# Kernel optimization log

Measured on AMD Instinct MI355X. Metric: run time of the kernel, lower is better.

Reference implementation:

```python
import jax, jax.numpy as jnp
import numpy as np

OUT = 7          # pooler output_size
RATIO = 2        # sampling_ratio
MIN_LEVEL, MAX_LEVEL = 2, 5
CANON_SIZE, CANON_LEVEL = 224.0, 4.0
SCALES = (0.25, 0.125, 0.0625, 0.03125)


def setup_inputs() -> dict:
    key = jax.random.key(0)
    ks = jax.random.split(key, 8)
    feat2 = jax.random.normal(ks[0], (2, 256, 200, 304), dtype=jnp.float32)
    feat3 = jax.random.normal(ks[1], (2, 256, 100, 152), dtype=jnp.float32)
    feat4 = jax.random.normal(ks[2], (2, 256, 50, 76), dtype=jnp.float32)
    feat5 = jax.random.normal(ks[3], (2, 256, 25, 38), dtype=jnp.float32)
    M = 1000
    imH, imW = 800.0, 1216.0
    cx = jax.random.uniform(ks[4], (M,)) * imW
    cy = jax.random.uniform(ks[5], (M,)) * imH
    wh = jax.random.uniform(ks[6], (M, 2)) * 400.0 + 8.0  # box sizes 8..408 px -> spans levels 2..5
    x0 = jnp.clip(cx - wh[:, 0] / 2, 0.0, imW - 1.0)
    x1 = jnp.clip(cx + wh[:, 0] / 2, 1.0, imW)
    y0 = jnp.clip(cy - wh[:, 1] / 2, 0.0, imH - 1.0)
    y1 = jnp.clip(cy + wh[:, 1] / 2, 1.0, imH)
    boxes = jnp.stack([x0, y0, x1, y1], axis=1).astype(jnp.float32)
    batch_idx = jax.random.randint(ks[7], (M,), 0, 2, dtype=jnp.int32)
    return {"feat2": feat2, "feat3": feat3, "feat4": feat4, "feat5": feat5,
            "boxes": boxes, "batch_idx": batch_idx}


def _assign_levels(boxes):
    # detectron2 assign_boxes_to_levels
    area = (boxes[:, 2] - boxes[:, 0]) * (boxes[:, 3] - boxes[:, 1])
    size = jnp.sqrt(area)
    lvl = jnp.floor(CANON_LEVEL + jnp.log2(size / CANON_SIZE + 1e-8))
    lvl = jnp.clip(lvl, MIN_LEVEL, MAX_LEVEL)
    return (lvl - MIN_LEVEL).astype(jnp.int32)  # [M] in 0..3


def _axis_weights(c, size):
    # torchvision roi_align bilinear clamping (per axis, separable)
    valid = ((c >= -1.0) & (c <= size)).astype(c.dtype)
    cc = jnp.maximum(c, 0.0)
    lo_f = jnp.floor(cc)
    cap = lo_f >= size - 1
    lo = jnp.where(cap, size - 1, lo_f).astype(jnp.int32)
    hi = jnp.where(cap, size - 1, lo + 1).astype(jnp.int32)
    l = jnp.where(cap, 0.0, cc - lo_f)
    return lo, hi, (1.0 - l) * valid, l * valid


def _roi_align(feat, boxes, bidx, scale):
    # feat [N,C,H,W], boxes [M,4] xyxy, aligned=True (ROIAlignV2)
    N, C, H, W = feat.shape
    M = boxes.shape[0]
    b = boxes * scale - 0.5  # aligned: shift by -0.5 after scaling
    x0, y0 = b[:, 0], b[:, 1]
    bin_w = (b[:, 2] - x0) / OUT
    bin_h = (b[:, 3] - y0) / OUT
    S = OUT * RATIO
    s = np.arange(S)
    offs = jnp.asarray((s // RATIO) + ((s % RATIO) + 0.5) / RATIO, dtype=feat.dtype)  # [S]
    ys = y0[:, None] + bin_h[:, None] * offs[None, :]  # [M,S]
    xs = x0[:, None] + bin_w[:, None] * offs[None, :]  # [M,S]
    ylo, yhi, wyl, wyh = _axis_weights(ys, H)
    xlo, xhi, wxl, wxh = _axis_weights(xs, W)

    def gather(yi, xi):
        # -> [M, S, S, C]
        return feat[bidx[:, None, None], :, yi[:, :, None], xi[:, None, :]]

    val = (gather(ylo, xlo) * (wyl[:, :, None] * wxl[:, None, :])[..., None]
         + gather(ylo, xhi) * (wyl[:, :, None] * wxh[:, None, :])[..., None]
         + gather(yhi, xlo) * (wyh[:, :, None] * wxl[:, None, :])[..., None]
         + gather(yhi, xhi) * (wyh[:, :, None] * wxh[:, None, :])[..., None])
    # average over the RATIOxRATIO sample subgrid of each output bin
    val = val.reshape(M, OUT, RATIO, OUT, RATIO, C).mean(axis=(2, 4))
    return val.transpose(0, 3, 1, 2)  # [M, C, OUT, OUT]


def reference(feat2, feat3, feat4, feat5, boxes, batch_idx):
    feats = (feat2, feat3, feat4, feat5)
    assign = _assign_levels(boxes)  # [M]
    M, C = boxes.shape[0], feat2.shape[1]
    out = jnp.zeros((M, C, OUT, OUT), dtype=feat2.dtype)
    for lvl, (f, sc) in enumerate(zip(feats, SCALES)):
        pooled = _roi_align(f, boxes, batch_idx, sc)
        out = out + pooled * (assign == lvl)[:, None, None, None].astype(out.dtype)
    return out
```

## Files before the change

### kernel.cpp

```cpp
#include <hip/hip_runtime.h>


#define NCH 256
#define POOL 7
#define NBIN 49
#define CAP 1152
#define WPB 4
#define TS 128

typedef __attribute__((address_space(3))) void       as3_void;
typedef __attribute__((address_space(1))) const void as1_void;

__global__ __launch_bounds__(256) void roi_precompute_kernel(
    const float* __restrict__ boxes, const int* __restrict__ bidx,
    unsigned int* __restrict__ tab, int M)
{
    const int lane = threadIdx.x & 63;
    const int m = blockIdx.x * WPB + (threadIdx.x >> 6);
    if (m >= M) return;

    float bx0 = boxes[4 * m + 0];
    float by0 = boxes[4 * m + 1];
    float bx1 = boxes[4 * m + 2];
    float by1 = boxes[4 * m + 3];

    float area = (bx1 - bx0) * (by1 - by0);
    float sz   = sqrtf(area);
    float lvlf = floorf(4.0f + log2f(sz / 224.0f + 1e-8f));
    lvlf = fminf(fmaxf(lvlf, 2.0f), 5.0f);
    int lvl = (int)lvlf - 2;

    int H, W; float scale;
    if (lvl == 0)      { H = 200; W = 304; scale = 0.25f;    }
    else if (lvl == 1) { H = 100; W = 152; scale = 0.125f;   }
    else if (lvl == 2) { H = 50;  W = 76;  scale = 0.0625f;  }
    else               { H = 25;  W = 38;  scale = 0.03125f; }

    float x0 = bx0 * scale - 0.5f;
    float y0 = by0 * scale - 0.5f;
    float bin_w = (bx1 * scale - 0.5f - x0) * (1.0f / 7.0f);
    float bin_h = (by1 * scale - 0.5f - y0) * (1.0f / 7.0f);

    int axis = lane >= 14;
    int s    = axis ? (lane - 14) : lane;
    float off = (float)(s >> 1) + ((s & 1) ? 0.75f : 0.25f);
    float cv    = axis ? (y0 + bin_h * off) : (x0 + bin_w * off);
    float size  = axis ? (float)H : (float)W;
    float valid = (cv >= -1.0f && cv <= size) ? 1.0f : 0.0f;
    float cc    = fmaxf(cv, 0.0f);
    float lo_f  = floorf(cc);
    bool  capd  = lo_f >= size - 1.0f;
    int   lo    = capd ? (int)size - 1 : (int)lo_f;
    int   hi    = capd ? lo : lo + 1;
    float l     = capd ? 0.0f : (cc - lo_f);
    float wlo   = (1.0f - l) * valid;
    float whi   = l * valid;

    int rx0 = __shfl(lo, 0);
    int rxe = __shfl(hi, 13);
    int ry0 = __shfl(lo, 14);
    int rye = __shfl(hi, 27);

    int FW  = rxe - rx0 + 1;
    int FH  = rye - ry0 + 1;
    int lpr = (FW + 3) >> 2;
    int RS4 = lpr << 2;
    int rpi = 64 / lpr;
    int iters = (FH + rpi - 1) / rpi;
    unsigned Mg  = (65536u   + (unsigned)lpr - 1u) / (unsigned)lpr;
    unsigned Mg2 = (4194304u + (unsigned)RS4 - 1u) / (unsigned)RS4;
    unsigned HW  = (unsigned)(H * W);
    unsigned base_off = (unsigned)bidx[m] * 256u * HW
                      + (unsigned)ry0 * (unsigned)W + (unsigned)rx0;
    int FH2 = FH;
    if (FH2 * RS4 > CAP) FH2 = CAP / RS4;
    unsigned lastoff = base_off + 255u * HW
                     + (unsigned)(FH - 1) * (unsigned)W + (unsigned)RS4;
    int safe = (lastoff <= 2u * 256u * HW) && (FH * RS4 <= CAP);

    unsigned* t = tab + (size_t)m * TS;
    if (lane == 0) {
        t[0]  = base_off;
        t[1]  = (unsigned)lvl;
        t[2]  = HW;
        t[3]  = (unsigned)W;
        t[4]  = (unsigned)lpr;
        t[5]  = Mg;
        t[6]  = (unsigned)rpi;
        t[7]  = (unsigned)iters;
        t[8]  = (unsigned)(rpi * W);
        t[9]  = (unsigned)((rpi * RS4) << 2);
        t[10] = (unsigned)((FH - 1) * W);
        t[11] = (unsigned)safe;
        t[12] = (unsigned)FW;
        t[13] = (unsigned)RS4;
        t[14] = (unsigned)FH2;
        t[15] = Mg2;
    }
    if (lane < 28) {
        if (!axis) {
            int xr = lo - rx0;
            int xp = min(xr + 1, FW - 1);
            uint4 v;
            v.x = (unsigned)xr;
            v.y = (unsigned)xp;
            v.z = __float_as_uint(wlo);
            v.w = __float_as_uint(whi);
            *(uint4*)(t + 16 + 4 * s) = v;
        } else {
            uint4 v;
            v.x = (unsigned)((lo - ry0) * RS4);
            v.y = (unsigned)((hi - ry0) * RS4);
            v.z = __float_as_uint(wlo);
            v.w = __float_as_uint(whi);
            *(uint4*)(t + 72 + 4 * s) = v;
        }
    }
}

__global__ __launch_bounds__(256, 8) void roi_align_kernel(
    const float* __restrict__ f0, const float* __restrict__ f1,
    const float* __restrict__ f2, const float* __restrict__ f3,
    const unsigned int* __restrict__ tab,
    float* __restrict__ out, int M)
{
    __shared__ float sF[WPB][CAP];

    const int lane = threadIdx.x & 63;
    const int w    = __builtin_amdgcn_readfirstlane(threadIdx.x >> 6);
    const int unit = blockIdx.x * WPB + w;
    if (unit >= M * NCH) return;
    const int m = unit >> 8;
    const int c = unit & (NCH - 1);

    const unsigned* t = tab + (size_t)m * TS;

    const int ci = lane < NBIN ? lane : 0;
    const int py = ci / POOL;
    const int px = ci - POOL * py;
    const uint4* xt = (const uint4*)(t + 16);
    const uint4* yt = (const uint4*)(t + 72);
    const uint4 X0 = xt[2 * px];
    const uint4 X1 = xt[2 * px + 1];
    const uint4 Y0 = yt[2 * py];
    const uint4 Y1 = yt[2 * py + 1];

    const uint4 s0 = *(const uint4*)(t);
    const uint4 s1 = *(const uint4*)(t + 4);
    const uint4 s2 = *(const uint4*)(t + 8);

    const int lvl = __builtin_amdgcn_readfirstlane((int)s0.y);
    const float* fp = (lvl == 0) ? f0 : (lvl == 1) ? f1 : (lvl == 2) ? f2 : f3;
    const unsigned HW = s0.z;
    const unsigned Wd = s0.w;
    const float* src = fp + (size_t)(s0.x + (unsigned)c * HW);

    const int safe = __builtin_amdgcn_readfirstlane((int)s2.w);
    if (safe) {
        const int lpr      = __builtin_amdgcn_readfirstlane((int)s1.x);
        const unsigned Mg  = s1.y;
        const int rpi      = __builtin_amdgcn_readfirstlane((int)s1.z);
        const int iters    = __builtin_amdgcn_readfirstlane((int)s1.w);
        const unsigned gstep  = s2.x;
        const unsigned lstepB = __builtin_amdgcn_readfirstlane((int)s2.y);
        const unsigned fhw    = s2.z;

        int sfy  = (int)(((unsigned)lane * Mg) >> 16);
        int sfx4 = (lane - sfy * lpr) << 2;
        if (sfy < rpi) {
            const float* g    = src + (unsigned)sfy * Wd + (unsigned)sfx4;
            const float* gmax = src + fhw + (unsigned)sfx4;
            char* lb = (char*)&sF[w][0];
            for (int it = 0; it < iters; ++it) {
                const float* gc = (g > gmax) ? gmax : g;
                __builtin_amdgcn_global_load_lds((as1_void*)gc,
                                                 (as3_void*)lb, 16, 0, 0);
                g  += gstep;
                lb += lstepB;
            }
        }
    } else {
        const uint4 s3 = *(const uint4*)(t + 12);
        const int FW  = __builtin_amdgcn_readfirstlane((int)s3.x);
        const int RS4 = __builtin_amdgcn_readfirstlane((int)s3.y);
        const int FH2 = __builtin_amdgcn_readfirstlane((int)s3.z);
        const unsigned Mg2 = s3.w;
        const int tot = FH2 * RS4;
        for (int i = lane; i < tot; i += 64) {
            int fy = (int)(((unsigned)i * Mg2) >> 22);
            int fx = i - fy * RS4;
            int cx = fx < FW ? fx : FW - 1;
            sF[w][i] = src[(unsigned)fy * Wd + (unsigned)cx];
        }
    }

    __builtin_amdgcn_s_waitcnt(0);
    __asm__ __volatile__("" ::: "memory");

    if (lane < NBIN) {
        const float* Fb = &sF[w][0];
        const unsigned xr0 = X0.x, xp0 = X0.y, xr1 = X1.x, xp1 = X1.y;
        const float wxl0 = __uint_as_float(X0.z), wxh0 = __uint_as_float(X0.w);
        const float wxl1 = __uint_as_float(X1.z), wxh1 = __uint_as_float(X1.w);
        const unsigned ra = Y0.x, rb = Y0.y, rc = Y1.x, rd = Y1.y;

        float a0 = Fb[ra + xr0] * wxl0 + Fb[ra + xp0] * wxh0
                 + Fb[ra + xr1] * wxl1 + Fb[ra + xp1] * wxh1;
        float a1 = Fb[rb + xr0] * wxl0 + Fb[rb + xp0] * wxh0
                 + Fb[rb + xr1] * wxl1 + Fb[rb + xp1] * wxh1;
        float a2 = Fb[rc + xr0] * wxl0 + Fb[rc + xp0] * wxh0
                 + Fb[rc + xr1] * wxl1 + Fb[rc + xp1] * wxh1;
        float a3 = Fb[rd + xr0] * wxl0 + Fb[rd + xp0] * wxh0
                 + Fb[rd + xr1] * wxl1 + Fb[rd + xp1] * wxh1;

        float acc = __uint_as_float(Y0.z) * a0 + __uint_as_float(Y0.w) * a1
                  + __uint_as_float(Y1.z) * a2 + __uint_as_float(Y1.w) * a3;

        out[(size_t)unit * NBIN + lane] = acc * 0.25f;
    }
}

extern "C" void kernel_launch(void* const* d_in, const int* in_sizes, int n_in,
                              void* d_out, int out_size, void* d_ws, size_t ws_size,
                              hipStream_t stream) {
    const float* f0    = (const float*)d_in[0];
    const float* f1    = (const float*)d_in[1];
    const float* f2    = (const float*)d_in[2];
    const float* f3    = (const float*)d_in[3];
    const float* boxes = (const float*)d_in[4];
    const int*   bidx  = (const int*)d_in[5];
    float* out = (float*)d_out;

    int M = in_sizes[4] / 4;
    unsigned int* tab = (unsigned int*)d_ws;

    int pblocks = (M + WPB - 1) / WPB;
    hipLaunchKernelGGL(roi_precompute_kernel, dim3(pblocks), dim3(256), 0,
                       stream, boxes, bidx, tab, M);

    int units = M * NCH;
    int blocks = (units + WPB - 1) / WPB;
    hipLaunchKernelGGL(roi_align_kernel, dim3(blocks), dim3(256), 0, stream,
                       f0, f1, f2, f3, tab, out, M);
}
```

Measured before the change: 292.8 us.

## Persistent double-buffered ROI pipeline with XCD-aware channel mapping and separate fallback kernel

Replaces the one-wave-per-(roi,channel) launch with a persistent grid of 1024 blocks. Each wave walks a contiguous chunk of ROIs for a fixed channel pair and double-buffers async global-to-LDS loads, so the next ROI is fetched while the current one is computed. Block indices are mapped so each XCD handles a fixed set of channels, aiming for L2 locality. ROIs that do not fit the fast path are put on an atomic list and handled by a separate fallback kernel that reads global memory directly. The cost is a memset and an extra launch, lower occupancy from 128-thread blocks with more LDS each, and dummy loads issued for unused pipeline slots.

```diff
diff --git a/kernel.cpp b/kernel.cpp
--- a/kernel.cpp
+++ b/kernel.cpp
@@ -5,18 +5,23 @@
 #define POOL 7
 #define NBIN 49
 #define CAP 1152
-#define WPB 4
-#define TS 128
+#define TS 160
+#define ITMAX 5
+#define PWPB 4
+#define DUMPF (4 * CAP)
+#define WREG (4 * CAP + 256)
 
 typedef __attribute__((address_space(3))) void       as3_void;
 typedef __attribute__((address_space(1))) const void as1_void;
+#define RFL(x) __builtin_amdgcn_readfirstlane(x)
 
 __global__ __launch_bounds__(256) void roi_precompute_kernel(
     const float* __restrict__ boxes, const int* __restrict__ bidx,
-    unsigned int* __restrict__ tab, int M)
+    unsigned int* __restrict__ tab, unsigned int* __restrict__ list,
+    unsigned int* __restrict__ cnt, int M)
 {
     const int lane = threadIdx.x & 63;
-    const int m = blockIdx.x * WPB + (threadIdx.x >> 6);
+    const int m = blockIdx.x * PWPB + (threadIdx.x >> 6);
     if (m >= M) return;
 
     float bx0 = boxes[4 * m + 0];
@@ -76,7 +81,9 @@
     if (FH2 * RS4 > CAP) FH2 = CAP / RS4;
     unsigned lastoff = base_off + 255u * HW
                      + (unsigned)(FH - 1) * (unsigned)W + (unsigned)RS4;
-    int safe = (lastoff <= 2u * 256u * HW) && (FH * RS4 <= CAP);
+    int safe = (lastoff <= 2u * 256u * HW)
+            && (iters * rpi * RS4 <= CAP)
+            && (iters <= ITMAX);
 
     unsigned* t = tab + (size_t)m * TS;
     if (lane == 0) {
@@ -96,6 +103,10 @@
         t[13] = (unsigned)RS4;
         t[14] = (unsigned)FH2;
         t[15] = Mg2;
+        if (!safe) {
+            unsigned i = atomicAdd(cnt, 1u);
+            list[i] = (unsigned)m;
+        }
     }
     if (lane < 28) {
         if (!axis) {
@@ -114,109 +125,238 @@
             v.z = __float_as_uint(wlo);
             v.w = __float_as_uint(whi);
             *(uint4*)(t + 72 + 4 * s) = v;
+            uint2 vw;
+            vw.x = (unsigned)((lo - ry0) * W);
+            vw.y = (unsigned)((hi - ry0) * W);
+            *(uint2*)(t + 128 + 2 * s) = vw;
         }
     }
 }
 
-__global__ __launch_bounds__(256, 8) void roi_align_kernel(
+#define STAGE(S0_, S1_, S2_, P_) do {                                        \
+    const int      lvl_   = RFL((int)(S0_).y);                               \
+    const float*   fp_    = (lvl_ == 0) ? f0 : (lvl_ == 1) ? f1              \
+                          : (lvl_ == 2) ? f2 : f3;                           \
+    const unsigned HW_    = (S0_).z;                                         \
+    const unsigned Wd_    = (S0_).w;                                         \
+    const int      safe_  = RFL((int)(S2_).w);                               \
+    const int      lpr_   = RFL((int)(S1_).x);                               \
+    const unsigned Mg_    = (S1_).y;                                         \
+    const int      rpi_   = RFL((int)(S1_).z);                               \
+    const int      iters_ = RFL((int)(S1_).w);                               \
+    const unsigned gstep_ = (S2_).x;                                         \
+    const unsigned lstep_ = (unsigned)RFL((int)(S2_).y);                     \
+    const unsigned fhw_   = (S2_).z;                                         \
+    const float*   src_   = fp_ + (size_t)((S0_).x + (unsigned)c0 * HW_);    \
+    int sfy_  = (int)(((unsigned)lane * Mg_) >> 16);                         \
+    int sfx4_ = (lane - sfy_ * lpr_) << 2;                                   \
+    if (sfy_ < rpi_) {                                                       \
+        const float* gA_  = src_ + (unsigned)sfy_ * Wd_ + (unsigned)sfx4_;   \
+        const float* gmA_ = src_ + fhw_ + (unsigned)sfx4_;                   \
+        const float* gB_  = gA_ + HW_;                                       \
+        const float* gmB_ = gmA_ + HW_;                                      \
+        char* lA_  = (char*)&sF[w][(P_) * 2 * CAP];                          \
+        char* lB_  = lA_ + CAP * 4;                                          \
+        char* dmp_ = (char*)&sF[w][DUMPF];                                   \
+        _Pragma("unroll")                                                    \
+        for (int it_ = 0; it_ < ITMAX; ++it_) {                              \
+            const float* pa_ = (gA_ > gmA_) ? gmA_ : gA_;                    \
+            const float* pb_ = (gB_ > gmB_) ? gmB_ : gB_;                    \
+            const float* qa_ = safe_ ? pa_ : (const float*)f0;               \
+            const float* qb_ = safe_ ? pb_ : (const float*)f0;               \
+            bool real_ = safe_ && (it_ < iters_);                            \
+            char* wa_ = real_ ? lA_ : dmp_;                                  \
+            char* wb_ = real_ ? lB_ : dmp_;                                  \
+            __builtin_amdgcn_global_load_lds((as1_void*)qa_,                 \
+                                             (as3_void*)wa_, 16, 0, 0);      \
+            __builtin_amdgcn_global_load_lds((as1_void*)qb_,                 \
+                                             (as3_void*)wb_, 16, 0, 0);      \
+            gA_ += gstep_; gB_ += gstep_; lA_ += lstep_; lB_ += lstep_;      \
+        }                                                                    \
+    }                                                                        \
+} while (0)
+
+#define GEOM(MM_, X0_, X1_, Y0_, Y1_, S0_, S1_, S2_) do {                    \
+    const unsigned* t_ = tab + (size_t)(MM_) * TS;                           \
+    const uint4* xt_ = (const uint4*)(t_ + 16);                              \
+    const uint4* yt_ = (const uint4*)(t_ + 72);                              \
+    X0_ = xt_[2 * px];  X1_ = xt_[2 * px + 1];                               \
+    Y0_ = yt_[2 * py];  Y1_ = yt_[2 * py + 1];                               \
+    S0_ = *(const uint4*)(t_);                                               \
+    S1_ = *(const uint4*)(t_ + 4);                                           \
+    S2_ = *(const uint4*)(t_ + 8);                                           \
+} while (0)
+
+#define COMPUTE_STORE(X0_, X1_, Y0_, Y1_, S2_, P_, M_) do {                  \
+    const int safe_ = RFL((int)(S2_).w);                                     \
+    if (safe_) {                                                             \
+        const float* FbA = &sF[w][(P_) * 2 * CAP];                           \
+        const float* FbB = FbA + CAP;                                        \
+        const unsigned xr0 = (X0_).x, xp0 = (X0_).y;                         \
+        const unsigned xr1 = (X1_).x, xp1 = (X1_).y;                         \
+        const float wxl0 = __uint_as_float((X0_).z);                         \
+        const float wxh0 = __uint_as_float((X0_).w);                         \
+        const float wxl1 = __uint_as_float((X1_).z);                         \
+        const float wxh1 = __uint_as_float((X1_).w);                         \
+        const unsigned ra = (Y0_).x, rb = (Y0_).y;                           \
+        const unsigned rc = (Y1_).x, rd = (Y1_).y;                           \
+        const float wy0 = __uint_as_float((Y0_).z);                          \
+        const float wy1 = __uint_as_float((Y0_).w);                          \
+        const float wy2 = __uint_as_float((Y1_).z);                          \
+        const float wy3 = __uint_as_float((Y1_).w);                          \
+        float a0 = FbA[ra + xr0] * wxl0 + FbA[ra + xp0] * wxh0               \
+                 + FbA[ra + xr1] * wxl1 + FbA[ra + xp1] * wxh1;              \
+        float a1 = FbA[rb + xr0] * wxl0 + FbA[rb + xp0] * wxh0               \
+                 + FbA[rb + xr1] * wxl1 + FbA[rb + xp1] * wxh1;              \
+        float a2 = FbA[rc + xr0] * wxl0 + FbA[rc + xp0] * wxh0               \
+                 + FbA[rc + xr1] * wxl1 + FbA[rc + xp1] * wxh1;              \
+        float a3 = FbA[rd + xr0] * wxl0 + FbA[rd + xp0] * wxh0               \
+                 + FbA[rd + xr1] * wxl1 + FbA[rd + xp1] * wxh1;              \
+        float accA = wy0 * a0 + wy1 * a1 + wy2 * a2 + wy3 * a3;              \
+        float b0 = FbB[ra + xr0] * wxl0 + FbB[ra + xp0] * wxh0               \
+                 + FbB[ra + xr1] * wxl1 + FbB[ra + xp1] * wxh1;              \
+        float b1 = FbB[rb + xr0] * wxl0 + FbB[rb + xp0] * wxh0               \
+                 + FbB[rb + xr1] * wxl1 + FbB[rb + xp1] * wxh1;              \
+        float b2 = FbB[rc + xr0] * wxl0 + FbB[rc + xp0] * wxh0               \
+                 + FbB[rc + xr1] * wxl1 + FbB[rc + xp1] * wxh1;              \
+        float b3 = FbB[rd + xr0] * wxl0 + FbB[rd + xp0] * wxh0               \
+                 + FbB[rd + xr1] * wxl1 + FbB[rd + xp1] * wxh1;              \
+        float accB = wy0 * b0 + wy1 * b1 + wy2 * b2 + wy3 * b3;              \
+        if (lane < NBIN) {                                                   \
+            size_t ob = ((size_t)(M_) * NCH + (unsigned)c0) * NBIN           \
+                      + (unsigned)lane;                                      \
+            out[ob]        = accA * 0.25f;                                   \
+            out[ob + NBIN] = accB * 0.25f;                                   \
+        }                                                                    \
+    }                                                                        \
+} while (0)
+
+#define WAIT10() do {                                                        \
+    __builtin_amdgcn_sched_barrier(0);                                       \
+    asm volatile("s_waitcnt vmcnt(10)" ::: "memory");                        \
+    __builtin_amdgcn_sched_barrier(0);                                       \
+} while (0)
+
+__global__ __launch_bounds__(128, 2) void roi_align_kernel(
     const float* __restrict__ f0, const float* __restrict__ f1,
     const float* __restrict__ f2, const float* __restrict__ f3,
     const unsigned int* __restrict__ tab,
     float* __restrict__ out, int M)
 {
-    __shared__ float sF[WPB][CAP];
+    __shared__ float sF[2][WREG];
 
     const int lane = threadIdx.x & 63;
     const int w    = __builtin_amdgcn_readfirstlane(threadIdx.x >> 6);
-    const int unit = blockIdx.x * WPB + w;
-    if (unit >= M * NCH) return;
-    const int m = unit >> 8;
-    const int c = unit & (NCH - 1);
-
-    const unsigned* t = tab + (size_t)m * TS;
+
+    const unsigned b        = blockIdx.x;
+    const unsigned xcd      = b & 7u;
+    const unsigned id       = b >> 3;
+    const unsigned cp_local = id >> 3;
+    const unsigned chpair   = id & 7u;
+    const int c0   = (int)((xcd * 16u + cp_local) * 2u);
+    const int CH   = (M + 15) >> 4;
+    const int chunk = (int)(chpair * 2u) + w;
+    const int m0   = chunk * CH;
+    const int mend = min(M, m0 + CH);
+    if (m0 >= mend) return;
 
     const int ci = lane < NBIN ? lane : 0;
     const int py = ci / POOL;
     const int px = ci - POOL * py;
-    const uint4* xt = (const uint4*)(t + 16);
-    const uint4* yt = (const uint4*)(t + 72);
-    const uint4 X0 = xt[2 * px];
-    const uint4 X1 = xt[2 * px + 1];
-    const uint4 Y0 = yt[2 * py];
-    const uint4 Y1 = yt[2 * py + 1];
-
-    const uint4 s0 = *(const uint4*)(t);
-    const uint4 s1 = *(const uint4*)(t + 4);
-    const uint4 s2 = *(const uint4*)(t + 8);
-
-    const int lvl = __builtin_amdgcn_readfirstlane((int)s0.y);
-    const float* fp = (lvl == 0) ? f0 : (lvl == 1) ? f1 : (lvl == 2) ? f2 : f3;
-    const unsigned HW = s0.z;
-    const unsigned Wd = s0.w;
-    const float* src = fp + (size_t)(s0.x + (unsigned)c * HW);
-
-    const int safe = __builtin_amdgcn_readfirstlane((int)s2.w);
-    if (safe) {
-        const int lpr      = __builtin_amdgcn_readfirstlane((int)s1.x);
-        const unsigned Mg  = s1.y;
-        const int rpi      = __builtin_amdgcn_readfirstlane((int)s1.z);
-        const int iters    = __builtin_amdgcn_readfirstlane((int)s1.w);
-        const unsigned gstep  = s2.x;
-        const unsigned lstepB = __builtin_amdgcn_readfirstlane((int)s2.y);
-        const unsigned fhw    = s2.z;
-
-        int sfy  = (int)(((unsigned)lane * Mg) >> 16);
-        int sfx4 = (lane - sfy * lpr) << 2;
-        if (sfy < rpi) {
-            const float* g    = src + (unsigned)sfy * Wd + (unsigned)sfx4;
-            const float* gmax = src + fhw + (unsigned)sfx4;
-            char* lb = (char*)&sF[w][0];
-            for (int it = 0; it < iters; ++it) {
-                const float* gc = (g > gmax) ? gmax : g;
-                __builtin_amdgcn_global_load_lds((as1_void*)gc,
-                                                 (as3_void*)lb, 16, 0, 0);
-                g  += gstep;
-                lb += lstepB;
-            }
-        }
-    } else {
-        const uint4 s3 = *(const uint4*)(t + 12);
-        const int FW  = __builtin_amdgcn_readfirstlane((int)s3.x);
-        const int RS4 = __builtin_amdgcn_readfirstlane((int)s3.y);
-        const int FH2 = __builtin_amdgcn_readfirstlane((int)s3.z);
-        const unsigned Mg2 = s3.w;
-        const int tot = FH2 * RS4;
-        for (int i = lane; i < tot; i += 64) {
-            int fy = (int)(((unsigned)i * Mg2) >> 22);
-            int fx = i - fy * RS4;
-            int cx = fx < FW ? fx : FW - 1;
-            sF[w][i] = src[(unsigned)fy * Wd + (unsigned)cx];
-        }
-    }
-
-    __builtin_amdgcn_s_waitcnt(0);
-    __asm__ __volatile__("" ::: "memory");
-
-    if (lane < NBIN) {
-        const float* Fb = &sF[w][0];
+
+    uint4 X0a, X1a, Y0a, Y1a, S0a, S1a, S2a;
+    uint4 X0b, X1b, Y0b, Y1b, S0b, S1b, S2b;
+
+    int m = m0;
+    GEOM(m, X0a, X1a, Y0a, Y1a, S0a, S1a, S2a);
+    STAGE(S0a, S1a, S2a, 0);
+    {
+        int m1 = (m + 1 < mend) ? m + 1 : m;
+        GEOM(m1, X0b, X1b, Y0b, Y1b, S0b, S1b, S2b);
+    }
+    int par = 0;
+
+    while (true) {
+        STAGE(S0b, S1b, S2b, par ^ 1);
+        WAIT10();
+        COMPUTE_STORE(X0a, X1a, Y0a, Y1a, S2a, par, m);
+        ++m; if (m >= mend) break;
+        par ^= 1;
+        {
+            int m2 = (m + 1 < mend) ? m + 1 : m;
+            GEOM(m2, X0a, X1a, Y0a, Y1a, S0a, S1a, S2a);
+        }
+        STAGE(S0a, S1a, S2a, par ^ 1);
+        WAIT10();
+        COMPUTE_STORE(X0b, X1b, Y0b, Y1b, S2b, par, m);
+        ++m; if (m >= mend) break;
+        par ^= 1;
+        {
+            int m2 = (m + 1 < mend) ? m + 1 : m;
+            GEOM(m2, X0b, X1b, Y0b, Y1b, S0b, S1b, S2b);
+        }
+    }
+    asm volatile("s_waitcnt vmcnt(0)" ::: "memory");
+}
+
+__global__ __launch_bounds__(256) void roi_fallback_kernel(
+    const float* __restrict__ f0, const float* __restrict__ f1,
+    const float* __restrict__ f2, const float* __restrict__ f3,
+    const unsigned int* __restrict__ tab, const unsigned int* __restrict__ list,
+    const unsigned int* __restrict__ cnt,
+    float* __restrict__ out, int M)
+{
+    const int lane = threadIdx.x & 63;
+    const unsigned wv = blockIdx.x * 4u + (threadIdx.x >> 6);
+    const unsigned nw = gridDim.x * 4u;
+    const unsigned total = cnt[0] * 256u;
+
+    const int ci = lane < NBIN ? lane : 0;
+    const int py = ci / POOL;
+    const int px = ci - POOL * py;
+
+    for (unsigned u = wv; u < total; u += nw) {
+        const unsigned mi = list[u >> 8];
+        const unsigned c  = u & 255u;
+        const unsigned* t = tab + (size_t)mi * TS;
+
+        const uint4 s0 = *(const uint4*)(t);
+        const int lvl = (int)s0.y;
+        const float* fp = (lvl == 0) ? f0 : (lvl == 1) ? f1
+                        : (lvl == 2) ? f2 : f3;
+        const float* src = fp + (size_t)(s0.x + c * s0.z);
+
+        const uint4* xt = (const uint4*)(t + 16);
+        const uint4* yt = (const uint4*)(t + 72);
+        const uint2* yw = (const uint2*)(t + 128);
+        const uint4 X0 = xt[2 * px];
+        const uint4 X1 = xt[2 * px + 1];
+        const uint4 Y0 = yt[2 * py];
+        const uint4 Y1 = yt[2 * py + 1];
+        const uint2 W0 = yw[2 * py];
+        const uint2 W1 = yw[2 * py + 1];
+
         const unsigned xr0 = X0.x, xp0 = X0.y, xr1 = X1.x, xp1 = X1.y;
         const float wxl0 = __uint_as_float(X0.z), wxh0 = __uint_as_float(X0.w);
         const float wxl1 = __uint_as_float(X1.z), wxh1 = __uint_as_float(X1.w);
-        const unsigned ra = Y0.x, rb = Y0.y, rc = Y1.x, rd = Y1.y;
-
-        float a0 = Fb[ra + xr0] * wxl0 + Fb[ra + xp0] * wxh0
-                 + Fb[ra + xr1] * wxl1 + Fb[ra + xp1] * wxh1;
-        float a1 = Fb[rb + xr0] * wxl0 + Fb[rb + xp0] * wxh0
-                 + Fb[rb + xr1] * wxl1 + Fb[rb + xp1] * wxh1;
-        float a2 = Fb[rc + xr0] * wxl0 + Fb[rc + xp0] * wxh0
-                 + Fb[rc + xr1] * wxl1 + Fb[rc + xp1] * wxh1;
-        float a3 = Fb[rd + xr0] * wxl0 + Fb[rd + xp0] * wxh0
-                 + Fb[rd + xr1] * wxl1 + Fb[rd + xp1] * wxh1;
-
-        float acc = __uint_as_float(Y0.z) * a0 + __uint_as_float(Y0.w) * a1
-                  + __uint_as_float(Y1.z) * a2 + __uint_as_float(Y1.w) * a3;
-
-        out[(size_t)unit * NBIN + lane] = acc * 0.25f;
+        const unsigned ra = W0.x, rb = W0.y, rc = W1.x, rd = W1.y;
+        const float wy0 = __uint_as_float(Y0.z), wy1 = __uint_as_float(Y0.w);
+        const float wy2 = __uint_as_float(Y1.z), wy3 = __uint_as_float(Y1.w);
+
+        float a0 = src[ra + xr0] * wxl0 + src[ra + xp0] * wxh0
+                 + src[ra + xr1] * wxl1 + src[ra + xp1] * wxh1;
+        float a1 = src[rb + xr0] * wxl0 + src[rb + xp0] * wxh0
+                 + src[rb + xr1] * wxl1 + src[rb + xp1] * wxh1;
+        float a2 = src[rc + xr0] * wxl0 + src[rc + xp0] * wxh0
+                 + src[rc + xr1] * wxl1 + src[rc + xp1] * wxh1;
+        float a3 = src[rd + xr0] * wxl0 + src[rd + xp0] * wxh0
+                 + src[rd + xr1] * wxl1 + src[rd + xp1] * wxh1;
+        float acc = wy0 * a0 + wy1 * a1 + wy2 * a2 + wy3 * a3;
+
+        if (lane < NBIN) {
+            size_t ob = ((size_t)mi * NCH + c) * NBIN + (unsigned)lane;
+            out[ob] = acc * 0.25f;
+        }
     }
 }
 
@@ -232,14 +372,19 @@
     float* out = (float*)d_out;
 
     int M = in_sizes[4] / 4;
-    unsigned int* tab = (unsigned int*)d_ws;
-
-    int pblocks = (M + WPB - 1) / WPB;
+    unsigned int* cnt  = (unsigned int*)d_ws;
+    unsigned int* list = cnt + 64;
+    unsigned int* tab  = cnt + 64 + 8192;
+
+    hipMemsetAsync(d_ws, 0, 4, stream);
+
+    int pblocks = (M + PWPB - 1) / PWPB;
     hipLaunchKernelGGL(roi_precompute_kernel, dim3(pblocks), dim3(256), 0,
-                       stream, boxes, bidx, tab, M);
-
-    int units = M * NCH;
-    int blocks = (units + WPB - 1) / WPB;
-    hipLaunchKernelGGL(roi_align_kernel, dim3(blocks), dim3(256), 0, stream,
+                       stream, boxes, bidx, tab, list, cnt, M);
+
+    hipLaunchKernelGGL(roi_align_kernel, dim3(1024), dim3(128), 0, stream,
                        f0, f1, f2, f3, tab, out, M);
+
+    hipLaunchKernelGGL(roi_fallback_kernel, dim3(128), dim3(256), 0, stream,
+                       f0, f1, f2, f3, tab, list, cnt, out, M);
 }
```

New measurement: 313.8 us. 7.2% more time.
